# Optimization experiments

Measured on AMD Instinct MI355X. Metric: run time of the kernel, lower is better.

The kernel has to match this reference:

```python
import jax, jax.numpy as jnp
import numpy as np

N = 100_000   # nodes
E = 1_600_000 # edges
NEG_SLOPE = 0.2

def _glorot(key, shape):
    fan = shape[0] + shape[-1]
    return jax.random.uniform(key, shape, jnp.float32, -1.0, 1.0) * np.sqrt(6.0 / fan)

def setup_inputs() -> dict:
    key = jax.random.key(0)
    ks = jax.random.split(key, 16)
    x = jax.random.normal(ks[0], (N, 2), jnp.float32)
    edge_index = jax.random.randint(ks[1], (2, E), 0, N)
    edge_weights = jax.random.uniform(ks[2], (E,), jnp.float32)
    # GATConv 1: in=2, out=32, heads=4, edge_dim=1 (lin/lin_edge have no bias in PyG)
    W1    = _glorot(ks[3], (2, 128))
    We1   = _glorot(ks[4], (1, 128))
    attS1 = _glorot(ks[5], (4, 32))
    attD1 = _glorot(ks[6], (4, 32))
    attE1 = _glorot(ks[7], (4, 32))
    b1    = jnp.zeros((128,), jnp.float32)
    # GATConv 2: in=128, out=1, heads=1, concat=False
    W2    = _glorot(ks[8], (128, 1))
    We2   = _glorot(ks[9], (1, 1))
    attS2 = _glorot(ks[10], (1, 1))
    attD2 = _glorot(ks[11], (1, 1))
    attE2 = _glorot(ks[12], (1, 1))
    b2    = jnp.zeros((1,), jnp.float32)
    return dict(x=x, edge_index=edge_index, edge_weights=edge_weights,
                W1=W1, attS1=attS1, attD1=attD1, We1=We1, attE1=attE1, b1=b1,
                W2=W2, attS2=attS2, attD2=attD2, We2=We2, attE2=attE2, b2=b2)

def _gat_layer(x, src, dst, eattr, W, We, a_s, a_d, a_e, b, heads, outc, concat):
    n = x.shape[0]
    # add self-loops; fill_value='mean' -> self-loop edge_attr = mean of incoming edge attrs
    cnt = jax.ops.segment_sum(jnp.ones((eattr.shape[0],), eattr.dtype), dst, num_segments=n)
    loop_attr = jax.ops.segment_sum(eattr, dst, num_segments=n) / jnp.maximum(cnt, 1.0)[:, None]
    loop = jnp.arange(n, dtype=src.dtype)
    src = jnp.concatenate([src, loop])
    dst = jnp.concatenate([dst, loop])
    ea = jnp.concatenate([eattr, loop_attr], axis=0)          # [E+N, edge_dim]
    h = (x @ W).reshape(n, heads, outc)                        # [N,H,C]
    a_src = jnp.sum(h * a_s, axis=-1)                          # [N,H]
    a_dst = jnp.sum(h * a_d, axis=-1)                          # [N,H]
    a_edge = jnp.sum((ea @ We).reshape(-1, heads, outc) * a_e, axis=-1)  # [E+N,H]
    logits = jax.nn.leaky_relu(a_src[src] + a_dst[dst] + a_edge, NEG_SLOPE)
    # scatter-softmax grouped by destination node
    m = jax.ops.segment_max(logits, dst, num_segments=n)       # every node has a self-loop
    p = jnp.exp(logits - m[dst])
    s = jax.ops.segment_sum(p, dst, num_segments=n)
    alpha = p / (s[dst] + 1e-16)                               # [E+N,H]
    out = jax.ops.segment_sum(h[src] * alpha[..., None], dst, num_segments=n)  # [N,H,C]
    out = out.reshape(n, heads * outc) if concat else out.mean(axis=1)
    return out + b

def reference(x, edge_index, edge_weights, W1, attS1, attD1, We1, attE1, b1,
              W2, attS2, attD2, We2, attE2, b2):
    src, dst = edge_index[0], edge_index[1]
    ea = edge_weights[:, None]  # edge_dim=1
    h = _gat_layer(x, src, dst, ea, W1, We1, attS1, attD1, attE1, b1, 4, 32, True)
    h = jax.nn.elu(h)
    out = _gat_layer(h, src, dst, ea, W2, We2, attS2, attD2, attE2, b2, 1, 1, False)
    return out.squeeze(-1)  # [N]
```

## Files before the change

kernel.cpp:

```cpp
#include <hip/hip_runtime.h>

#define N_NODES 100000
#define N_EDGES 1600000
#define NQUAD (N_EDGES / 4)
#define NEG_SLOPE 0.2f

#define NBKT 512
#define BDIV 196
#define NUSED 511
#define PB 500
#define QPB (NQUAD / PB)
#define PBS 512
#define BCAP 4096

typedef int   vint4   __attribute__((ext_vector_type(4)));
typedef float vfloat4 __attribute__((ext_vector_type(4)));

__device__ __forceinline__ float leaky(float v) { return v >= 0.f ? v : NEG_SLOPE * v; }

__global__ void __launch_bounds__(256) k_hist(const int* __restrict__ ei,
                                              int* __restrict__ histT) {
    __shared__ int hist[NBKT];
    int tid = threadIdx.x;
    hist[tid] = 0;
    hist[tid + 256] = 0;
    __syncthreads();
    const vint4* dst4 = (const vint4*)(ei + N_EDGES);
    int q0 = blockIdx.x * QPB;
    for (int q = tid; q < QPB; q += 256) {
        vint4 d = __builtin_nontemporal_load(&dst4[q0 + q]);
        atomicAdd(&hist[d.x / BDIV], 1);
        atomicAdd(&hist[d.y / BDIV], 1);
        atomicAdd(&hist[d.z / BDIV], 1);
        atomicAdd(&hist[d.w / BDIV], 1);
    }
    __syncthreads();
    histT[tid * PBS + blockIdx.x] = hist[tid];
    histT[(tid + 256) * PBS + blockIdx.x] = hist[tid + 256];
}

__global__ void __launch_bounds__(512) k_rowscan(const int* __restrict__ histT,
                                                 int* __restrict__ offT,
                                                 int* __restrict__ btot) {
    __shared__ int sm[512];
    int b = blockIdx.x, tid = threadIdx.x;
    int v = (tid < PB) ? histT[b * PBS + tid] : 0;
    sm[tid] = v;
    __syncthreads();
    for (int off = 1; off < 512; off <<= 1) {
        int t = (tid >= off) ? sm[tid - off] : 0;
        __syncthreads();
        sm[tid] += t;
        __syncthreads();
    }
    if (tid < PB) offT[b * PBS + tid] = sm[tid] - v;
    if (tid == 511) btot[b] = sm[511];
}

__global__ void __launch_bounds__(512) k_bprefix(const int* __restrict__ btot,
                                                 int* __restrict__ bbase,
                                                 int* __restrict__ bcnt,
                                                 const float* __restrict__ W1,
                                                 const float* __restrict__ attS1,
                                                 const float* __restrict__ attD1,
                                                 const float* __restrict__ We1,
                                                 const float* __restrict__ attE1,
                                                 float* __restrict__ consts) {
    __shared__ int sm[512];
    int tid = threadIdx.x;
    if (tid < 8) {
        int r = tid >> 2, h = tid & 3;
        float s = 0.f;
        for (int c = 0; c < 32; ++c) s += W1[r * 128 + h * 32 + c] * attS1[h * 32 + c];
        consts[tid] = s;
    } else if (tid < 16) {
        int u = tid - 8, r = u >> 2, h = u & 3;
        float s = 0.f;
        for (int c = 0; c < 32; ++c) s += W1[r * 128 + h * 32 + c] * attD1[h * 32 + c];
        consts[tid] = s;
    } else if (tid < 20) {
        int h = tid - 16;
        float s = 0.f;
        for (int c = 0; c < 32; ++c) s += We1[h * 32 + c] * attE1[h * 32 + c];
        consts[tid] = s;
    }
    int v = btot[tid];
    sm[tid] = v;
    __syncthreads();
    for (int off = 1; off < 512; off <<= 1) {
        int t = (tid >= off) ? sm[tid - off] : 0;
        __syncthreads();
        sm[tid] += t;
        __syncthreads();
    }
    bbase[tid] = sm[tid] - v;
    bcnt[tid] = v;
}

__global__ void __launch_bounds__(512) k_part(const int* __restrict__ ei,
                                              const float* __restrict__ w,
                                              const int* __restrict__ offT,
                                              const int* __restrict__ bbase,
                                              const float* __restrict__ x,
                                              vint4* __restrict__ staging) {
    __shared__ int lcur[NBKT];
    int tid = threadIdx.x;
    lcur[tid] = offT[tid * PBS + blockIdx.x] + bbase[tid];
    __syncthreads();
    const vint4* src4 = (const vint4*)ei;
    const vint4* dst4 = (const vint4*)(ei + N_EDGES);
    const vfloat4* w4 = (const vfloat4*)w;
    int q0 = blockIdx.x * QPB;
    for (int q = tid; q < QPB; q += 512) {
        vint4 s = __builtin_nontemporal_load(&src4[q0 + q]);
        vint4 d = __builtin_nontemporal_load(&dst4[q0 + q]);
        vfloat4 ww = __builtin_nontemporal_load(&w4[q0 + q]);
#pragma unroll
        for (int j = 0; j < 4; ++j) {
            int dd = (j == 0) ? d.x : (j == 1) ? d.y : (j == 2) ? d.z : d.w;
            int ss = (j == 0) ? s.x : (j == 1) ? s.y : (j == 2) ? s.z : s.w;
            float wv = (j == 0) ? ww.x : (j == 1) ? ww.y : (j == 2) ? ww.z : ww.w;
            int b = dd / BDIV;
            int pos = atomicAdd(&lcur[b], 1);
            float2 xs = *(const float2*)(x + 2 * ss);
            vint4 r = {ss | ((dd - b * BDIV) << 17), __float_as_int(wv),
                       __float_as_int(xs.x), __float_as_int(xs.y)};
            staging[pos] = r;
        }
    }
}

__global__ void __launch_bounds__(512) k_build(const int* __restrict__ bbase,
                                               const int* __restrict__ bcnt,
                                               vint4* __restrict__ staging,
                                               int* __restrict__ deg,
                                               int* __restrict__ rowst) {
    __shared__ vint4 seg[BCAP];
    __shared__ int hist[256];
    __shared__ int lcur[BDIV];
    int b = blockIdx.x, tid = threadIdx.x;
    int base = bbase[b];
    int cnt = min(bcnt[b], BCAP);
    if (tid < 256) hist[tid] = 0;
    __syncthreads();
    for (int i = tid; i < cnt; i += 512) {
        vint4 r = staging[base + i];
        seg[i] = r;
        atomicAdd(&hist[r.x >> 17], 1);
    }
    __syncthreads();
    int v = (tid < 256) ? hist[tid] : 0;
    for (int off = 1; off < 256; off <<= 1) {
        int t = (tid < 256 && tid >= off) ? hist[tid - off] : 0;
        __syncthreads();
        if (tid < 256) hist[tid] += t;
        __syncthreads();
    }
    int n0 = b * BDIV;
    int nnode = min(BDIV, N_NODES - n0);
    if (tid < nnode) {
        deg[n0 + tid] = v;
        rowst[n0 + tid] = base + hist[tid] - v;
    }
    if (tid < BDIV) lcur[tid] = hist[tid] - v;
    __syncthreads();
    for (int i = tid; i < cnt; i += 512) {
        vint4 r = seg[i];
        int pos = atomicAdd(&lcur[r.x >> 17], 1);
        staging[base + pos] = r;
    }
}

__global__ void __launch_bounds__(256) k_gather1(const int* __restrict__ deg,
                                                 const int* __restrict__ rowst,
                                                 const vint4* __restrict__ csr,
                                                 const float* __restrict__ x,
                                                 const float* __restrict__ consts,
                                                 const float* __restrict__ W1,
                                                 const float* __restrict__ b1,
                                                 const float* __restrict__ W2,
                                                 float* __restrict__ h2,
                                                 float* __restrict__ la) {
    __shared__ float w10[132], w11[132], b1s[132], w2s[132];
    for (int j = threadIdx.x; j < 128; j += blockDim.x) {
        int jj = (j >> 5) * 33 + (j & 31);
        w10[jj] = W1[j];
        w11[jj] = W1[128 + j];
        b1s[jj] = b1[j];
        w2s[jj] = W2[j];
    }
    __syncthreads();
    int t = blockIdx.x * blockDim.x + threadIdx.x;
    int n = t >> 3, l = t & 7;
    if (n >= N_NODES) return;
    float c[20];
#pragma unroll
    for (int i = 0; i < 20; ++i) c[i] = consts[i];
    int rs = rowst[n], d = deg[n];
    float2 xn = *(const float2*)(x + 2 * n);
    float adv[4];
#pragma unroll
    for (int h = 0; h < 4; ++h) adv[h] = xn.x * c[8 + h] + xn.y * c[12 + h];
    float s[4] = {0, 0, 0, 0}, X0[4] = {0, 0, 0, 0}, X1[4] = {0, 0, 0, 0};
    float wsum = 0.f;
    for (int k = rs + l; k < rs + d; k += 8) {
        vint4 r = csr[k];
        float wt = __int_as_float(r.y);
        float x0s = __int_as_float(r.z), x1s = __int_as_float(r.w);
        wsum += wt;
#pragma unroll
        for (int h = 0; h < 4; ++h) {
            float as = x0s * c[h] + x1s * c[4 + h];
            float p = __expf(leaky(as + adv[h] + wt * c[16 + h]));
            s[h] += p;
            X0[h] += p * x0s;
            X1[h] += p * x1s;
        }
    }
#pragma unroll
    for (int off = 1; off < 8; off <<= 1) {
        wsum += __shfl_xor(wsum, off);
#pragma unroll
        for (int h = 0; h < 4; ++h) {
            s[h]  += __shfl_xor(s[h], off);
            X0[h] += __shfl_xor(X0[h], off);
            X1[h] += __shfl_xor(X1[h], off);
        }
    }
    float lav = wsum / fmaxf((float)d, 1.f);
#pragma unroll
    for (int h = 0; h < 4; ++h) {
        float aso = xn.x * c[h] + xn.y * c[4 + h];
        float p = __expf(leaky(aso + adv[h] + lav * c[16 + h]));
        s[h] += p;
        X0[h] += p * xn.x;
        X1[h] += p * xn.y;
    }
    int hh = l & 3;
    float sh  = (hh == 0) ? s[0]  : (hh == 1) ? s[1]  : (hh == 2) ? s[2]  : s[3];
    float X0h = (hh == 0) ? X0[0] : (hh == 1) ? X0[1] : (hh == 2) ? X0[2] : X0[3];
    float X1h = (hh == 0) ? X1[0] : (hh == 1) ? X1[1] : (hh == 2) ? X1[2] : X1[3];
    float inv = 1.f / (sh + 1e-16f);
    X0h *= inv;
    X1h *= inv;
    float acc = 0.f;
    int basej = hh * 33 + (l >> 2) * 16;
    for (int cc = 0; cc < 16; ++cc) {
        float v = X0h * w10[basej + cc] + X1h * w11[basej + cc] + b1s[basej + cc];
        float el = v > 0.f ? v : __expf(v) - 1.f;
        acc += el * w2s[basej + cc];
    }
    acc += __shfl_xor(acc, 1);
    acc += __shfl_xor(acc, 2);
    acc += __shfl_xor(acc, 4);
    if (l == 0) {
        h2[n] = acc;
        la[n] = lav;
    }
}

__global__ void __launch_bounds__(256) k_gather2(const int* __restrict__ deg,
                                                 const int* __restrict__ rowst,
                                                 const vint4* __restrict__ csr,
                                                 const float* __restrict__ h2,
                                                 const float* __restrict__ la,
                                                 const float* __restrict__ attS2,
                                                 const float* __restrict__ attD2,
                                                 const float* __restrict__ We2,
                                                 const float* __restrict__ attE2,
                                                 const float* __restrict__ b2,
                                                 float* __restrict__ out) {
    int t = blockIdx.x * blockDim.x + threadIdx.x;
    int n = t >> 3, l = t & 7;
    if (n >= N_NODES) return;
    float aS = attS2[0], aD = attD2[0], cE = We2[0] * attE2[0], bb = b2[0];
    int rs = rowst[n], d = deg[n];
    float hn = h2[n];
    float hnaD = hn * aD;
    float s = 0.f, acc = 0.f;
    for (int k = rs + l; k < rs + d; k += 8) {
        vint4 r = csr[k];
        float hs = h2[r.x & 0x1FFFF];
        float wt = __int_as_float(r.y);
        float p = __expf(leaky(hs * aS + hnaD + wt * cE));
        s += p;
        acc += p * hs;
    }
#pragma unroll
    for (int off = 1; off < 8; off <<= 1) {
        s   += __shfl_xor(s, off);
        acc += __shfl_xor(acc, off);
    }
    float p = __expf(leaky(hn * aS + hnaD + la[n] * cE));
    s += p;
    acc += p * hn;
    if (l == 0) out[n] = acc / (s + 1e-16f) + bb;
}

extern "C" void kernel_launch(void* const* d_in, const int* in_sizes, int n_in,
                              void* d_out, int out_size, void* d_ws, size_t ws_size,
                              hipStream_t stream) {
    const float* x     = (const float*)d_in[0];
    const int*   ei    = (const int*)d_in[1];
    const float* w     = (const float*)d_in[2];
    const float* W1    = (const float*)d_in[3];
    const float* attS1 = (const float*)d_in[4];
    const float* attD1 = (const float*)d_in[5];
    const float* We1   = (const float*)d_in[6];
    const float* attE1 = (const float*)d_in[7];
    const float* b1    = (const float*)d_in[8];
    const float* W2    = (const float*)d_in[9];
    const float* attS2 = (const float*)d_in[10];
    const float* attD2 = (const float*)d_in[11];
    const float* We2   = (const float*)d_in[12];
    const float* attE2 = (const float*)d_in[13];
    const float* b2    = (const float*)d_in[14];
    float* out = (float*)d_out;

    const size_t N = N_NODES;

    int*   histT   = (int*)d_ws;
    int*   offT    = histT + NBKT * PBS;
    int*   btot    = offT + NBKT * PBS;
    int*   bbase   = btot + NBKT;
    int*   bcnt    = bbase + NBKT;
    float* consts  = (float*)(bcnt + NBKT);
    vint4* staging = (vint4*)(consts + 32);
    int*   deg     = (int*)(staging + N_EDGES);
    int*   rowst   = deg + N;
    float* h2      = (float*)(rowst + N);
    float* la      = h2 + N;

    k_hist<<<PB, 256, 0, stream>>>(ei, histT);
    k_rowscan<<<NBKT, 512, 0, stream>>>(histT, offT, btot);
    k_bprefix<<<1, 512, 0, stream>>>(btot, bbase, bcnt, W1, attS1, attD1, We1,
                                     attE1, consts);
    k_part<<<PB, 512, 0, stream>>>(ei, w, offT, bbase, x, staging);
    k_build<<<NUSED, 512, 0, stream>>>(bbase, bcnt, staging, deg, rowst);
    k_gather1<<<(8 * N_NODES + 255) / 256, 256, 0, stream>>>(deg, rowst, staging, x,
                                                             consts, W1, b1, W2, h2, la);
    k_gather2<<<(8 * N_NODES + 255) / 256, 256, 0, stream>>>(deg, rowst, staging, h2, la,
                                                             attS2, attD2, We2, attE2,
                                                             b2, out);
}
```

Before: 176.6 us.

## Fuse CSR build with layer-1 gather in shared memory, emit compact int2 CSR

Merges the bucket build kernel with the first GAT layer's gather. Each block sorts its bucket's edges into shared-memory arrays and computes layer-1 attention and the output projection for its nodes straight from LDS. This removes the global write-back of the 16-byte sorted records and their re-read in a separate kernel. It also writes a compact 8-byte (src, weight) CSR for layer 2, halving that kernel's edge-stream traffic. The cost is much higher shared-memory use per block (about 112 KB), which limits occupancy, and layer-1 compute is now spread over only 511 blocks.

```diff
diff --git a/kernel.cpp b/kernel.cpp
--- a/kernel.cpp
+++ b/kernel.cpp
@@ -130,18 +130,32 @@
     }
 }
 
-__global__ void __launch_bounds__(512) k_build(const int* __restrict__ bbase,
-                                               const int* __restrict__ bcnt,
-                                               vint4* __restrict__ staging,
-                                               int* __restrict__ deg,
-                                               int* __restrict__ rowst) {
+__global__ void __launch_bounds__(512) k_bg1(const int* __restrict__ bbase,
+                                             const int* __restrict__ bcnt,
+                                             const vint4* __restrict__ staging,
+                                             int2* __restrict__ csr2,
+                                             const float* __restrict__ x,
+                                             const float* __restrict__ consts,
+                                             const float* __restrict__ W1,
+                                             const float* __restrict__ b1,
+                                             const float* __restrict__ W2,
+                                             int* __restrict__ deg,
+                                             int* __restrict__ rowst,
+                                             float* __restrict__ h2,
+                                             float* __restrict__ la) {
     __shared__ vint4 seg[BCAP];
+    __shared__ float sw[BCAP], sx0[BCAP], sx1[BCAP];
     __shared__ int hist[256];
-    __shared__ int lcur[BDIV];
+    __shared__ int lcur[BDIV], rowloc[BDIV], degL[BDIV];
+    __shared__ float w10[132], w11[132], b1s[132], w2s[132];
     int b = blockIdx.x, tid = threadIdx.x;
     int base = bbase[b];
     int cnt = min(bcnt[b], BCAP);
     if (tid < 256) hist[tid] = 0;
+    for (int j = tid; j < 128; j += 512) {
+        int jj = (j >> 5) * 33 + (j & 31);
+        w10[jj] = W1[j]; w11[jj] = W1[128 + j]; b1s[jj] = b1[j]; w2s[jj] = W2[j];
+    }
     __syncthreads();
     for (int i = tid; i < cnt; i += 512) {
         vint4 r = staging[base + i];
@@ -161,107 +175,92 @@
     if (tid < nnode) {
         deg[n0 + tid] = v;
         rowst[n0 + tid] = base + hist[tid] - v;
-    }
-    if (tid < BDIV) lcur[tid] = hist[tid] - v;
+        degL[tid] = v;
+        rowloc[tid] = hist[tid] - v;
+        lcur[tid] = hist[tid] - v;
+    }
     __syncthreads();
     for (int i = tid; i < cnt; i += 512) {
         vint4 r = seg[i];
-        int pos = atomicAdd(&lcur[r.x >> 17], 1);
-        staging[base + pos] = r;
-    }
-}
-
-__global__ void __launch_bounds__(256) k_gather1(const int* __restrict__ deg,
-                                                 const int* __restrict__ rowst,
-                                                 const vint4* __restrict__ csr,
-                                                 const float* __restrict__ x,
-                                                 const float* __restrict__ consts,
-                                                 const float* __restrict__ W1,
-                                                 const float* __restrict__ b1,
-                                                 const float* __restrict__ W2,
-                                                 float* __restrict__ h2,
-                                                 float* __restrict__ la) {
-    __shared__ float w10[132], w11[132], b1s[132], w2s[132];
-    for (int j = threadIdx.x; j < 128; j += blockDim.x) {
-        int jj = (j >> 5) * 33 + (j & 31);
-        w10[jj] = W1[j];
-        w11[jj] = W1[128 + j];
-        b1s[jj] = b1[j];
-        w2s[jj] = W2[j];
-    }
-    __syncthreads();
-    int t = blockIdx.x * blockDim.x + threadIdx.x;
-    int n = t >> 3, l = t & 7;
-    if (n >= N_NODES) return;
+        int dl = r.x >> 17;
+        int pos = atomicAdd(&lcur[dl], 1);
+        sw[pos] = __int_as_float(r.y);
+        sx0[pos] = __int_as_float(r.z);
+        sx1[pos] = __int_as_float(r.w);
+        csr2[base + pos] = make_int2(r.x & 0x1FFFF, r.y);
+    }
+    __syncthreads();
     float c[20];
 #pragma unroll
     for (int i = 0; i < 20; ++i) c[i] = consts[i];
-    int rs = rowst[n], d = deg[n];
-    float2 xn = *(const float2*)(x + 2 * n);
-    float adv[4];
-#pragma unroll
-    for (int h = 0; h < 4; ++h) adv[h] = xn.x * c[8 + h] + xn.y * c[12 + h];
-    float s[4] = {0, 0, 0, 0}, X0[4] = {0, 0, 0, 0}, X1[4] = {0, 0, 0, 0};
-    float wsum = 0.f;
-    for (int k = rs + l; k < rs + d; k += 8) {
-        vint4 r = csr[k];
-        float wt = __int_as_float(r.y);
-        float x0s = __int_as_float(r.z), x1s = __int_as_float(r.w);
-        wsum += wt;
+    int g = tid >> 3, l = tid & 7;
+    for (int j = g; j < nnode; j += 64) {
+        int n = n0 + j;
+        int rsL = rowloc[j], d = degL[j];
+        float2 xn = *(const float2*)(x + 2 * n);
+        float adv[4];
+#pragma unroll
+        for (int h = 0; h < 4; ++h) adv[h] = xn.x * c[8 + h] + xn.y * c[12 + h];
+        float s[4] = {0, 0, 0, 0}, X0[4] = {0, 0, 0, 0}, X1[4] = {0, 0, 0, 0};
+        float wsum = 0.f;
+        for (int k = rsL + l; k < rsL + d; k += 8) {
+            float wt = sw[k], x0s = sx0[k], x1s = sx1[k];
+            wsum += wt;
+#pragma unroll
+            for (int h = 0; h < 4; ++h) {
+                float as = x0s * c[h] + x1s * c[4 + h];
+                float p = __expf(leaky(as + adv[h] + wt * c[16 + h]));
+                s[h] += p;
+                X0[h] += p * x0s;
+                X1[h] += p * x1s;
+            }
+        }
+#pragma unroll
+        for (int off = 1; off < 8; off <<= 1) {
+            wsum += __shfl_xor(wsum, off);
+#pragma unroll
+            for (int h = 0; h < 4; ++h) {
+                s[h]  += __shfl_xor(s[h], off);
+                X0[h] += __shfl_xor(X0[h], off);
+                X1[h] += __shfl_xor(X1[h], off);
+            }
+        }
+        float lav = wsum / fmaxf((float)d, 1.f);
 #pragma unroll
         for (int h = 0; h < 4; ++h) {
-            float as = x0s * c[h] + x1s * c[4 + h];
-            float p = __expf(leaky(as + adv[h] + wt * c[16 + h]));
+            float aso = xn.x * c[h] + xn.y * c[4 + h];
+            float p = __expf(leaky(aso + adv[h] + lav * c[16 + h]));
             s[h] += p;
-            X0[h] += p * x0s;
-            X1[h] += p * x1s;
-        }
-    }
-#pragma unroll
-    for (int off = 1; off < 8; off <<= 1) {
-        wsum += __shfl_xor(wsum, off);
-#pragma unroll
-        for (int h = 0; h < 4; ++h) {
-            s[h]  += __shfl_xor(s[h], off);
-            X0[h] += __shfl_xor(X0[h], off);
-            X1[h] += __shfl_xor(X1[h], off);
-        }
-    }
-    float lav = wsum / fmaxf((float)d, 1.f);
-#pragma unroll
-    for (int h = 0; h < 4; ++h) {
-        float aso = xn.x * c[h] + xn.y * c[4 + h];
-        float p = __expf(leaky(aso + adv[h] + lav * c[16 + h]));
-        s[h] += p;
-        X0[h] += p * xn.x;
-        X1[h] += p * xn.y;
-    }
-    int hh = l & 3;
-    float sh  = (hh == 0) ? s[0]  : (hh == 1) ? s[1]  : (hh == 2) ? s[2]  : s[3];
-    float X0h = (hh == 0) ? X0[0] : (hh == 1) ? X0[1] : (hh == 2) ? X0[2] : X0[3];
-    float X1h = (hh == 0) ? X1[0] : (hh == 1) ? X1[1] : (hh == 2) ? X1[2] : X1[3];
-    float inv = 1.f / (sh + 1e-16f);
-    X0h *= inv;
-    X1h *= inv;
-    float acc = 0.f;
-    int basej = hh * 33 + (l >> 2) * 16;
-    for (int cc = 0; cc < 16; ++cc) {
-        float v = X0h * w10[basej + cc] + X1h * w11[basej + cc] + b1s[basej + cc];
-        float el = v > 0.f ? v : __expf(v) - 1.f;
-        acc += el * w2s[basej + cc];
-    }
-    acc += __shfl_xor(acc, 1);
-    acc += __shfl_xor(acc, 2);
-    acc += __shfl_xor(acc, 4);
-    if (l == 0) {
-        h2[n] = acc;
-        la[n] = lav;
+            X0[h] += p * xn.x;
+            X1[h] += p * xn.y;
+        }
+        int hh = l & 3;
+        float sh  = (hh == 0) ? s[0]  : (hh == 1) ? s[1]  : (hh == 2) ? s[2]  : s[3];
+        float X0h = (hh == 0) ? X0[0] : (hh == 1) ? X0[1] : (hh == 2) ? X0[2] : X0[3];
+        float X1h = (hh == 0) ? X1[0] : (hh == 1) ? X1[1] : (hh == 2) ? X1[2] : X1[3];
+        float inv = 1.f / (sh + 1e-16f);
+        X0h *= inv;
+        X1h *= inv;
+        float acc = 0.f;
+        int basej = hh * 33 + (l >> 2) * 16;
+        for (int cc = 0; cc < 16; ++cc) {
+            float vv = X0h * w10[basej + cc] + X1h * w11[basej + cc] + b1s[basej + cc];
+            float el = vv > 0.f ? vv : __expf(vv) - 1.f;
+            acc += el * w2s[basej + cc];
+        }
+        acc += __shfl_xor(acc, 1);
+        acc += __shfl_xor(acc, 2);
+        acc += __shfl_xor(acc, 4);
+        if (l == 0) {
+            h2[n] = acc;
+            la[n] = lav;
+        }
     }
 }
 
 __global__ void __launch_bounds__(256) k_gather2(const int* __restrict__ deg,
                                                  const int* __restrict__ rowst,
-                                                 const vint4* __restrict__ csr,
+                                                 const int2* __restrict__ csr2,
                                                  const float* __restrict__ h2,
                                                  const float* __restrict__ la,
                                                  const float* __restrict__ attS2,
@@ -279,8 +278,8 @@
     float hnaD = hn * aD;
     float s = 0.f, acc = 0.f;
     for (int k = rs + l; k < rs + d; k += 8) {
-        vint4 r = csr[k];
-        float hs = h2[r.x & 0x1FFFF];
+        int2 r = csr2[k];
+        float hs = h2[r.x];
         float wt = __int_as_float(r.y);
         float p = __expf(leaky(hs * aS + hnaD + wt * cE));
         s += p;
@@ -326,7 +325,8 @@
     int*   bcnt    = bbase + NBKT;
     float* consts  = (float*)(bcnt + NBKT);
     vint4* staging = (vint4*)(consts + 32);
-    int*   deg     = (int*)(staging + N_EDGES);
+    int2*  csr2    = (int2*)(staging + N_EDGES);
+    int*   deg     = (int*)(csr2 + N_EDGES);
     int*   rowst   = deg + N;
     float* h2      = (float*)(rowst + N);
     float* la      = h2 + N;
@@ -336,10 +336,9 @@
     k_bprefix<<<1, 512, 0, stream>>>(btot, bbase, bcnt, W1, attS1, attD1, We1,
                                      attE1, consts);
     k_part<<<PB, 512, 0, stream>>>(ei, w, offT, bbase, x, staging);
-    k_build<<<NUSED, 512, 0, stream>>>(bbase, bcnt, staging, deg, rowst);
-    k_gather1<<<(8 * N_NODES + 255) / 256, 256, 0, stream>>>(deg, rowst, staging, x,
-                                                             consts, W1, b1, W2, h2, la);
-    k_gather2<<<(8 * N_NODES + 255) / 256, 256, 0, stream>>>(deg, rowst, staging, h2, la,
+    k_bg1<<<NUSED, 512, 0, stream>>>(bbase, bcnt, staging, csr2, x, consts,
+                                     W1, b1, W2, deg, rowst, h2, la);
+    k_gather2<<<(8 * N_NODES + 255) / 256, 256, 0, stream>>>(deg, rowst, csr2, h2, la,
                                                              attS2, attD2, We2, attE2,
                                                              b2, out);
 }
```

New measurement: 179.8 us. Within noise of the previous version (+1.8%).
